# Optimization experiments

Hardware: AMD Instinct MI355X
Metric: run time of the kernel (lower is better)

Reference implementation:

```python
import jax, jax.numpy as jnp
import numpy as np

ND_WEIGHT = 1.0
NUM_CLASS = 1000
B, D = 16384, 2048


def setup_inputs() -> dict:
    key = jax.random.key(0)
    k1, k2, k3, k4 = jax.random.split(key, 4)
    s_emb = jax.random.normal(k1, (B, D), dtype=jnp.float32)
    t_emb = jax.random.normal(k2, (B, D), dtype=jnp.float32)
    T_EMB = jax.random.normal(k3, (NUM_CLASS, D), dtype=jnp.float32)
    labels = jax.random.randint(k4, (B,), 0, NUM_CLASS, dtype=jnp.int64)
    return {"s_emb": s_emb, "t_emb": t_emb, "T_EMB": T_EMB, "labels": labels}


def reference(s_emb, t_emb, T_EMB, labels):
    # Gather per-sample class centers: [B, D]
    centers = T_EMB[labels]
    # Unit-normalize each center (L2 along feature dim)
    e_c = centers / jnp.linalg.norm(centers, axis=-1, keepdims=True)
    # Per-sample max of student/teacher embedding norms: [B]
    s_norm = jnp.linalg.norm(s_emb, axis=-1)
    t_norm = jnp.linalg.norm(t_emb, axis=-1)
    max_norm = jnp.maximum(s_norm, t_norm)
    # 1 - <s, e_c> / max_norm, summed then averaged, scaled by nd_weight
    dots = jnp.sum(s_emb * e_c, axis=-1)
    loss_sum = jnp.sum(1.0 - dots / max_norm)
    return loss_sum * ND_WEIGHT / s_emb.shape[0]
```

## Files before the change

### kernel.cpp

```cpp
#include <hip/hip_runtime.h>


#define NROWS      16384
#define DDIM       2048
#define BLK        256
#define GRID       1024
#define NUM_WAVES  (GRID * (BLK / 64))

__global__ __launch_bounds__(BLK) void dnl_main_kernel(
    const float* __restrict__ s_emb,
    const float* __restrict__ t_emb,
    const float* __restrict__ T_EMB,
    const int*   __restrict__ labels,
    float*       __restrict__ wavesum)
{
    const int tid   = threadIdx.x;
    const int lane  = tid & 63;
    const int gwave = blockIdx.x * (BLK / 64) + (tid >> 6);

    float acc = 0.f;
    int next_label = labels[gwave];

    for (int row = gwave; row < NROWS; row += NUM_WAVES) {
        const int label = next_label;
        const int nrow  = row + NUM_WAVES;
        if (nrow < NROWS) next_label = labels[nrow];

        const float4* s4 = (const float4*)(s_emb + (size_t)row   * DDIM);
        const float4* t4 = (const float4*)(t_emb + (size_t)row   * DDIM);
        const float4* c4 = (const float4*)(T_EMB + (size_t)label * DDIM);

        float ss = 0.f, tt = 0.f, sc = 0.f, cc = 0.f;
        #pragma unroll
        for (int j = 0; j < 8; ++j) {
            const int k = lane + j * 64;
            const float4 s = s4[k];
            const float4 t = t4[k];
            const float4 c = c4[k];
            ss += s.x*s.x + s.y*s.y + s.z*s.z + s.w*s.w;
            tt += t.x*t.x + t.y*t.y + t.z*t.z + t.w*t.w;
            sc += s.x*c.x + s.y*c.y + s.z*c.z + s.w*c.w;
            cc += c.x*c.x + c.y*c.y + c.z*c.z + c.w*c.w;
        }

        #pragma unroll
        for (int off = 32; off > 0; off >>= 1) {
            ss += __shfl_xor(ss, off, 64);
            tt += __shfl_xor(tt, off, 64);
            sc += __shfl_xor(sc, off, 64);
            cc += __shfl_xor(cc, off, 64);
        }

        const float max_norm = fmaxf(sqrtf(ss), sqrtf(tt));
        acc += 1.0f - sc / (sqrtf(cc) * max_norm);
    }

    if (lane == 0) wavesum[gwave] = acc;
}

__global__ __launch_bounds__(BLK) void dnl_reduce_kernel(
    const float* __restrict__ wavesum,
    float*       __restrict__ out)
{
    const int tid = threadIdx.x;
    const float4* w4 = (const float4*)wavesum;
    float sum = 0.f;
    #pragma unroll
    for (int j = 0; j < 4; ++j) {
        const float4 v = w4[tid + j * BLK];
        sum += v.x + v.y + v.z + v.w;
    }

    #pragma unroll
    for (int off = 32; off > 0; off >>= 1)
        sum += __shfl_xor(sum, off, 64);

    __shared__ float red[4];
    if ((tid & 63) == 0) red[tid >> 6] = sum;
    __syncthreads();
    if (tid == 0)
        out[0] = (red[0] + red[1] + red[2] + red[3]) * (1.0f / (float)NROWS);
}

__global__ __launch_bounds__(BLK) void dnl_main_atomic_kernel(
    const float* __restrict__ s_emb,
    const float* __restrict__ t_emb,
    const float* __restrict__ T_EMB,
    const int*   __restrict__ labels,
    float*       __restrict__ out)
{
    const int tid   = threadIdx.x;
    const int lane  = tid & 63;
    const int gwave = blockIdx.x * (BLK / 64) + (tid >> 6);

    float acc = 0.f;
    for (int row = gwave; row < NROWS; row += NUM_WAVES) {
        const int label = labels[row];
        const float4* s4 = (const float4*)(s_emb + (size_t)row   * DDIM);
        const float4* t4 = (const float4*)(t_emb + (size_t)row   * DDIM);
        const float4* c4 = (const float4*)(T_EMB + (size_t)label * DDIM);
        float ss = 0.f, tt = 0.f, sc = 0.f, cc = 0.f;
        #pragma unroll
        for (int j = 0; j < 8; ++j) {
            const int k = lane + j * 64;
            const float4 s = s4[k];
            const float4 t = t4[k];
            const float4 c = c4[k];
            ss += s.x*s.x + s.y*s.y + s.z*s.z + s.w*s.w;
            tt += t.x*t.x + t.y*t.y + t.z*t.z + t.w*t.w;
            sc += s.x*c.x + s.y*c.y + s.z*c.z + s.w*c.w;
            cc += c.x*c.x + c.y*c.y + c.z*c.z + c.w*c.w;
        }
        #pragma unroll
        for (int off = 32; off > 0; off >>= 1) {
            ss += __shfl_xor(ss, off, 64);
            tt += __shfl_xor(tt, off, 64);
            sc += __shfl_xor(sc, off, 64);
            cc += __shfl_xor(cc, off, 64);
        }
        const float max_norm = fmaxf(sqrtf(ss), sqrtf(tt));
        acc += 1.0f - sc / (sqrtf(cc) * max_norm);
    }
    if (lane == 0) atomicAdd(out, acc * (1.0f / (float)NROWS));
}

extern "C" void kernel_launch(void* const* d_in, const int* in_sizes, int n_in,
                              void* d_out, int out_size, void* d_ws, size_t ws_size,
                              hipStream_t stream) {
    const float* s_emb  = (const float*)d_in[0];
    const float* t_emb  = (const float*)d_in[1];
    const float* T_EMB  = (const float*)d_in[2];
    const int*   labels = (const int*)d_in[3];
    float* out = (float*)d_out;

    if (ws_size >= (size_t)NUM_WAVES * sizeof(float)) {
        float* wavesum = (float*)d_ws;
        dnl_main_kernel<<<GRID, BLK, 0, stream>>>(s_emb, t_emb, T_EMB, labels, wavesum);
        dnl_reduce_kernel<<<1, BLK, 0, stream>>>(wavesum, out);
    } else {
        hipMemsetAsync(d_out, 0, sizeof(float), stream);
        dnl_main_atomic_kernel<<<GRID, BLK, 0, stream>>>(s_emb, t_emb, T_EMB, labels, out);
    }
}
```

Baseline: 287.9 us.

## Assign one row per wave and issue all row loads up front

Replaces the grid-stride loop over rows with one wave per row, launching 4096 blocks of 4 waves. Each lane loads all 24 float4 values for s, t and the class center into registers before doing any arithmetic, so many loads are in flight at once. Per-row losses go to a 16384-entry buffer that the reduce kernel sums. This costs more registers per thread and more block launches, and the reduce kernel now reads four times as many partials.

```diff
diff --git a/kernel.cpp b/kernel.cpp
--- a/kernel.cpp
+++ b/kernel.cpp
@@ -1,73 +1,71 @@
 #include <hip/hip_runtime.h>
 
 
-#define NROWS      16384
-#define DDIM       2048
-#define BLK        256
-#define GRID       1024
-#define NUM_WAVES  (GRID * (BLK / 64))
+#define NROWS  16384
+#define DDIM   2048
+#define BLK    256
+#define WPB    (BLK / 64)
+#define GRID   (NROWS / WPB)
 
-__global__ __launch_bounds__(BLK) void dnl_main_kernel(
+__global__ __launch_bounds__(BLK, 2) void dnl_main_kernel(
     const float* __restrict__ s_emb,
     const float* __restrict__ t_emb,
     const float* __restrict__ T_EMB,
     const int*   __restrict__ labels,
-    float*       __restrict__ wavesum)
+    float*       __restrict__ partial)
 {
-    const int tid   = threadIdx.x;
-    const int lane  = tid & 63;
-    const int gwave = blockIdx.x * (BLK / 64) + (tid >> 6);
+    const int tid  = threadIdx.x;
+    const int lane = tid & 63;
+    const int row  = blockIdx.x * WPB + (tid >> 6);
 
-    float acc = 0.f;
-    int next_label = labels[gwave];
+    const int label = labels[row];
 
-    for (int row = gwave; row < NROWS; row += NUM_WAVES) {
-        const int label = next_label;
-        const int nrow  = row + NUM_WAVES;
-        if (nrow < NROWS) next_label = labels[nrow];
+    const float4* s4 = (const float4*)(s_emb + (size_t)row   * DDIM);
+    const float4* t4 = (const float4*)(t_emb + (size_t)row   * DDIM);
+    const float4* c4 = (const float4*)(T_EMB + (size_t)label * DDIM);
 
-        const float4* s4 = (const float4*)(s_emb + (size_t)row   * DDIM);
-        const float4* t4 = (const float4*)(t_emb + (size_t)row   * DDIM);
-        const float4* c4 = (const float4*)(T_EMB + (size_t)label * DDIM);
+    float4 sv[8], tv[8], cv[8];
+    #pragma unroll
+    for (int j = 0; j < 8; ++j) sv[j] = s4[lane + j * 64];
+    #pragma unroll
+    for (int j = 0; j < 8; ++j) tv[j] = t4[lane + j * 64];
+    #pragma unroll
+    for (int j = 0; j < 8; ++j) cv[j] = c4[lane + j * 64];
 
-        float ss = 0.f, tt = 0.f, sc = 0.f, cc = 0.f;
-        #pragma unroll
-        for (int j = 0; j < 8; ++j) {
-            const int k = lane + j * 64;
-            const float4 s = s4[k];
-            const float4 t = t4[k];
-            const float4 c = c4[k];
-            ss += s.x*s.x + s.y*s.y + s.z*s.z + s.w*s.w;
-            tt += t.x*t.x + t.y*t.y + t.z*t.z + t.w*t.w;
-            sc += s.x*c.x + s.y*c.y + s.z*c.z + s.w*c.w;
-            cc += c.x*c.x + c.y*c.y + c.z*c.z + c.w*c.w;
-        }
-
-        #pragma unroll
-        for (int off = 32; off > 0; off >>= 1) {
-            ss += __shfl_xor(ss, off, 64);
-            tt += __shfl_xor(tt, off, 64);
-            sc += __shfl_xor(sc, off, 64);
-            cc += __shfl_xor(cc, off, 64);
-        }
-
-        const float max_norm = fmaxf(sqrtf(ss), sqrtf(tt));
-        acc += 1.0f - sc / (sqrtf(cc) * max_norm);
+    float ss = 0.f, tt = 0.f, sc = 0.f, cc = 0.f;
+    #pragma unroll
+    for (int j = 0; j < 8; ++j) {
+        const float4 s = sv[j], t = tv[j], c = cv[j];
+        ss += s.x*s.x + s.y*s.y + s.z*s.z + s.w*s.w;
+        tt += t.x*t.x + t.y*t.y + t.z*t.z + t.w*t.w;
+        sc += s.x*c.x + s.y*c.y + s.z*c.z + s.w*c.w;
+        cc += c.x*c.x + c.y*c.y + c.z*c.z + c.w*c.w;
     }
 
-    if (lane == 0) wavesum[gwave] = acc;
+    #pragma unroll
+    for (int off = 32; off > 0; off >>= 1) {
+        ss += __shfl_xor(ss, off, 64);
+        tt += __shfl_xor(tt, off, 64);
+        sc += __shfl_xor(sc, off, 64);
+        cc += __shfl_xor(cc, off, 64);
+    }
+
+    if (lane == 0) {
+        const float max_norm = fmaxf(sqrtf(ss), sqrtf(tt));
+        partial[row] = 1.0f - sc / (sqrtf(cc) * max_norm);
+    }
 }
 
 __global__ __launch_bounds__(BLK) void dnl_reduce_kernel(
-    const float* __restrict__ wavesum,
+    const float* __restrict__ partial,
     float*       __restrict__ out)
 {
     const int tid = threadIdx.x;
-    const float4* w4 = (const float4*)wavesum;
+    const float4* p4 = (const float4*)partial;
     float sum = 0.f;
     #pragma unroll
-    for (int j = 0; j < 4; ++j) {
-        const float4 v = w4[tid + j * BLK];
+    for (int j = 0; j < 16; ++j) {
+        const float4 v = p4[tid + j * BLK];
         sum += v.x + v.y + v.z + v.w;
     }
 
@@ -82,46 +80,50 @@
         out[0] = (red[0] + red[1] + red[2] + red[3]) * (1.0f / (float)NROWS);
 }
 
-__global__ __launch_bounds__(BLK) void dnl_main_atomic_kernel(
+__global__ __launch_bounds__(BLK, 2) void dnl_main_atomic_kernel(
     const float* __restrict__ s_emb,
     const float* __restrict__ t_emb,
     const float* __restrict__ T_EMB,
     const int*   __restrict__ labels,
     float*       __restrict__ out)
 {
-    const int tid   = threadIdx.x;
-    const int lane  = tid & 63;
-    const int gwave = blockIdx.x * (BLK / 64) + (tid >> 6);
+    const int tid  = threadIdx.x;
+    const int lane = tid & 63;
+    const int row  = blockIdx.x * WPB + (tid >> 6);
+    const int label = labels[row];
 
-    float acc = 0.f;
-    for (int row = gwave; row < NROWS; row += NUM_WAVES) {
-        const int label = labels[row];
-        const float4* s4 = (const float4*)(s_emb + (size_t)row   * DDIM);
-        const float4* t4 = (const float4*)(t_emb + (size_t)row   * DDIM);
-        const float4* c4 = (const float4*)(T_EMB + (size_t)label * DDIM);
-        float ss = 0.f, tt = 0.f, sc = 0.f, cc = 0.f;
-        #pragma unroll
-        for (int j = 0; j < 8; ++j) {
-            const int k = lane + j * 64;
-            const float4 s = s4[k];
-            const float4 t = t4[k];
-            const float4 c = c4[k];
-            ss += s.x*s.x + s.y*s.y + s.z*s.z + s.w*s.w;
-            tt += t.x*t.x + t.y*t.y + t.z*t.z + t.w*t.w;
-            sc += s.x*c.x + s.y*c.y + s.z*c.z + s.w*c.w;
-            cc += c.x*c.x + c.y*c.y + c.z*c.z + c.w*c.w;
-        }
-        #pragma unroll
-        for (int off = 32; off > 0; off >>= 1) {
-            ss += __shfl_xor(ss, off, 64);
-            tt += __shfl_xor(tt, off, 64);
-            sc += __shfl_xor(sc, off, 64);
-            cc += __shfl_xor(cc, off, 64);
-        }
+    const float4* s4 = (const float4*)(s_emb + (size_t)row   * DDIM);
+    const float4* t4 = (const float4*)(t_emb + (size_t)row   * DDIM);
+    const float4* c4 = (const float4*)(T_EMB + (size_t)label * DDIM);
+
+    float4 sv[8], tv[8], cv[8];
+    #pragma unroll
+    for (int j = 0; j < 8; ++j) sv[j] = s4[lane + j * 64];
+    #pragma unroll
+    for (int j = 0; j < 8; ++j) tv[j] = t4[lane + j * 64];
+    #pragma unroll
+    for (int j = 0; j < 8; ++j) cv[j] = c4[lane + j * 64];
+
+    float ss = 0.f, tt = 0.f, sc = 0.f, cc = 0.f;
+    #pragma unroll
+    for (int j = 0; j < 8; ++j) {
+        const float4 s = sv[j], t = tv[j], c = cv[j];
+        ss += s.x*s.x + s.y*s.y + s.z*s.z + s.w*s.w;
+        tt += t.x*t.x + t.y*t.y + t.z*t.z + t.w*t.w;
+        sc += s.x*c.x + s.y*c.y + s.z*c.z + s.w*c.w;
+        cc += c.x*c.x + c.y*c.y + c.z*c.z + c.w*c.w;
+    }
+    #pragma unroll
+    for (int off = 32; off > 0; off >>= 1) {
+        ss += __shfl_xor(ss, off, 64);
+        tt += __shfl_xor(tt, off, 64);
+        sc += __shfl_xor(sc, off, 64);
+        cc += __shfl_xor(cc, off, 64);
+    }
+    if (lane == 0) {
         const float max_norm = fmaxf(sqrtf(ss), sqrtf(tt));
-        acc += 1.0f - sc / (sqrtf(cc) * max_norm);
+        atomicAdd(out, (1.0f - sc / (sqrtf(cc) * max_norm)) * (1.0f / (float)NROWS));
     }
-    if (lane == 0) atomicAdd(out, acc * (1.0f / (float)NROWS));
 }
 
 extern "C" void kernel_launch(void* const* d_in, const int* in_sizes, int n_in,
@@ -133,10 +135,10 @@
     const int*   labels = (const int*)d_in[3];
     float* out = (float*)d_out;
 
-    if (ws_size >= (size_t)NUM_WAVES * sizeof(float)) {
-        float* wavesum = (float*)d_ws;
-        dnl_main_kernel<<<GRID, BLK, 0, stream>>>(s_emb, t_emb, T_EMB, labels, wavesum);
-        dnl_reduce_kernel<<<1, BLK, 0, stream>>>(wavesum, out);
+    if (ws_size >= (size_t)NROWS * sizeof(float)) {
+        float* partial = (float*)d_ws;
+        dnl_main_kernel<<<GRID, BLK, 0, stream>>>(s_emb, t_emb, T_EMB, labels, partial);
+        dnl_reduce_kernel<<<1, BLK, 0, stream>>>(partial, out);
     } else {
         hipMemsetAsync(d_out, 0, sizeof(float), stream);
         dnl_main_atomic_kernel<<<GRID, BLK, 0, stream>>>(s_emb, t_emb, T_EMB, labels, out);
```

Result: no change. 287.7 us (-0.1%).
